# Kernel optimization log

Hardware: AMD Instinct MI355X
Metric: run time of the kernel (lower is better)

The kernel has to match this reference:

```python
import jax, jax.numpy as jnp
import numpy as np

N_NODES = 50000
N_EDGES = 800000
IN, HID, OUT = 512, 256, 128


def spmm(edge_src, edge_dst, edge_weight, x, n_nodes):
    # y[i] = sum_{e: dst[e]==i} w[e] * x[src[e]]   (sparse adjacency @ x)
    msgs = edge_weight[:, None] * x[edge_src]          # [E, F] gather
    return jax.ops.segment_sum(msgs, edge_dst, num_segments=n_nodes)


def setup_inputs() -> dict:
    key = jax.random.key(0)
    k1, k2, k3, k4, k5, k6 = jax.random.split(key, 6)
    features = jax.random.normal(k1, (N_NODES, IN), dtype=jnp.float32)
    edge_src = jax.random.randint(k2, (N_EDGES,), 0, N_NODES, dtype=jnp.int32)
    edge_dst = jax.random.randint(k3, (N_EDGES,), 0, N_NODES, dtype=jnp.int32)
    edge_weight = jax.random.uniform(k4, (N_EDGES,), dtype=jnp.float32)
    # init like torch: uniform(-stdv, stdv), stdv = 1/sqrt(out_dim)
    s1 = 1.0 / np.sqrt(HID)
    s2 = 1.0 / np.sqrt(OUT)
    W1 = jax.random.uniform(k5, (IN, HID), dtype=jnp.float32, minval=-s1, maxval=s1)
    W2 = jax.random.uniform(k6, (HID, OUT), dtype=jnp.float32, minval=-s2, maxval=s2)
    return {"features": features, "edge_src": edge_src, "edge_dst": edge_dst,
            "edge_weight": edge_weight, "W1": W1, "W2": W2}


def reference(features, edge_src, edge_dst, edge_weight, W1, W2):
    n = features.shape[0]
    # layer 1: dense GEMM -> SpMM -> ReLU
    hidden = jax.nn.relu(spmm(edge_src, edge_dst, edge_weight, features @ W1, n))
    # layer 2: dense GEMM -> SpMM
    out = spmm(edge_src, edge_dst, edge_weight, hidden @ W2, n)
    return out
```

## Files before the change

### kernel.cpp

```cpp
#include <hip/hip_runtime.h>

#define NN 50000
#define NE 800000
#define FIN 512
#define FHID 256
#define FOUT 128
#define MPAD 50048

#define TW1_BLOCKS  512
#define TW2_BLOCKS  128

#define NBKT   196
#define BCAP   5120
#define BSTRIDE 16
#define PA_BLOCKS 392
#define E_CHA    2048
#define PB_BLOCKS 196

using bf16x8 = __attribute__((ext_vector_type(8))) short;
using f32x4  = __attribute__((ext_vector_type(4))) float;
using u16x8  = __attribute__((ext_vector_type(8))) unsigned short;

__device__ __forceinline__ unsigned short f2bf(float f) {
    unsigned int u = __builtin_bit_cast(unsigned int, f);
    unsigned int r = (u + 0x7FFFu + ((u >> 16) & 1u)) >> 16;
    return (unsigned short)r;
}
__device__ __forceinline__ float bf2f(unsigned short u) {
    return __builtin_bit_cast(float, (unsigned int)u << 16);
}
__device__ __forceinline__ void gload_lds16(const void* g, void* l) {
    __builtin_amdgcn_global_load_lds(
        (const __attribute__((address_space(1))) void*)g,
        (__attribute__((address_space(3))) void*)l, 16, 0, 0);
}


__global__ __launch_bounds__(256) void fused_passa_prep_kernel(
    const int* __restrict__ src, const int* __restrict__ dst,
    const float* __restrict__ w, int* __restrict__ bcur, int2* __restrict__ barr,
    const float* __restrict__ W1, unsigned short* __restrict__ W1T,
    const float* __restrict__ W2, unsigned short* __restrict__ W2T) {
    int b = blockIdx.x, tid = threadIdx.x;
    if (b < PA_BLOCKS) {
        __shared__ int hist[NBKT];
        __shared__ int resv[NBKT];
        if (tid < NBKT) hist[tid] = 0;
        __syncthreads();
        int base = b * E_CHA + tid;
        int  d[8];
        bool m[8];
#pragma unroll
        for (int j = 0; j < 8; ++j) {
            int e = base + j * 256;
            m[j] = e < NE;
            d[j] = m[j] ? dst[e] : 0;
        }
#pragma unroll
        for (int j = 0; j < 8; ++j)
            if (m[j]) atomicAdd(&hist[d[j] >> 8], 1);
        __syncthreads();
        if (tid < NBKT) {
            int h = hist[tid];
            resv[tid] = (h > 0) ? atomicAdd(&bcur[tid * BSTRIDE], h) : 0;
            hist[tid] = 0;
        }
        __syncthreads();
        int   s[8];
        float wv[8];
#pragma unroll
        for (int j = 0; j < 8; ++j) {
            int e = base + j * 256;
            s[j]  = m[j] ? src[e] : 0;
            wv[j] = m[j] ? w[e] : 0.f;
        }
#pragma unroll
        for (int j = 0; j < 8; ++j) {
            if (m[j]) {
                int bb = d[j] >> 8;
                int r  = atomicAdd(&hist[bb], 1);
                int pos = resv[bb] + r;
                if (pos < BCAP)
                    barr[(size_t)bb * BCAP + pos] =
                        make_int2(s[j] | ((d[j] & 255) << 16), __float_as_int(wv[j]));
            }
        }
    } else if (b < PA_BLOCKS + TW1_BLOCKS) {
        int t = (b - PA_BLOCKS) * 256 + tid;
        int n = t % FHID, k = t / FHID;
        W1T[(size_t)n * FIN + k] = f2bf(W1[t]);
    } else {
        int t = (b - PA_BLOCKS - TW1_BLOCKS) * 256 + tid;
        int n = t % FOUT, k = t / FOUT;
        W2T[(size_t)n * FHID + k] = f2bf(W2[t]);
    }
}


__device__ __forceinline__ void gemm1_body(const float* __restrict__ X,
                                           const unsigned short* __restrict__ BT,
                                           unsigned short* __restrict__ C,
                                           int bx) {
    __shared__ unsigned short As[64 * 64];
    __shared__ unsigned short Bs[256 * 64];

    const int tid  = threadIdx.x;
    const int lane = tid & 63;
    const int wid  = tid >> 6;
    const int brow = bx * 64;
    const int r15   = lane & 15;
    const int khalf = (lane >> 4) * 8;

    const int arow0 = tid >> 3;
    const int arow1 = 32 + (tid >> 3);
    const int acol  = (tid & 7) * 8;
    const int g0 = min(brow + arow0, NN - 1);
    const int g1 = min(brow + arow1, NN - 1);
    const float4* ap0 = (const float4*)(X + (size_t)g0 * FIN + acol);
    const float4* ap1 = (const float4*)(X + (size_t)g1 * FIN + acol);
    const int ab0 = arow0 * 128 + ((acol * 2) ^ ((arow0 & 7) << 4));
    const int ab1 = arow1 * 128 + ((acol * 2) ^ ((arow1 & 7) << 4));

    f32x4 acc[4][4] = {};
    float4 a00 = ap0[0], a01 = ap0[1], a10 = ap1[0], a11 = ap1[1];

#pragma unroll
    for (int k = 0; k < 8; ++k) {
        const int k0 = k * 64;
#pragma unroll
        for (int c = 0; c < 8; ++c) {
            int b   = wid * 8192 + c * 1024 + lane * 16;
            int row = b >> 7;
            int cby = (b & 127) ^ ((row & 7) << 4);
            const char* gb = (const char*)(BT + (size_t)row * FIN + k0) + cby;
            gload_lds16(gb, (char*)Bs + wid * 8192 + c * 1024);
        }
        {
            u16x8 v;
            v[0] = f2bf(a00.x); v[1] = f2bf(a00.y); v[2] = f2bf(a00.z); v[3] = f2bf(a00.w);
            v[4] = f2bf(a01.x); v[5] = f2bf(a01.y); v[6] = f2bf(a01.z); v[7] = f2bf(a01.w);
            *(u16x8*)((char*)As + ab0) = v;
            v[0] = f2bf(a10.x); v[1] = f2bf(a10.y); v[2] = f2bf(a10.z); v[3] = f2bf(a10.w);
            v[4] = f2bf(a11.x); v[5] = f2bf(a11.y); v[6] = f2bf(a11.z); v[7] = f2bf(a11.w);
            *(u16x8*)((char*)As + ab1) = v;
        }
        __syncthreads();

        if (k < 7) {
            int q = (k0 + 64) >> 2;
            a00 = ap0[q]; a01 = ap0[q + 1]; a10 = ap1[q]; a11 = ap1[q + 1];
        }

        bf16x8 bfr[4][2];
#pragma unroll
        for (int n = 0; n < 4; ++n) {
            int row = wid * 64 + n * 16 + r15;
            int rb  = row * 128;
            int sw  = (row & 7) << 4;
#pragma unroll
            for (int ks = 0; ks < 2; ++ks)
                bfr[n][ks] = *(const bf16x8*)((const char*)Bs + rb + (((ks * 32 + khalf) * 2) ^ sw));
        }
#pragma unroll
        for (int m = 0; m < 4; ++m) {
            int row = m * 16 + r15;
            int rb  = row * 128;
            int sw  = (row & 7) << 4;
            bf16x8 af0 = *(const bf16x8*)((const char*)As + rb + (((0 + khalf) * 2) ^ sw));
            bf16x8 af1 = *(const bf16x8*)((const char*)As + rb + (((32 + khalf) * 2) ^ sw));
#pragma unroll
            for (int n = 0; n < 4; ++n) {
                acc[m][n] = __builtin_amdgcn_mfma_f32_16x16x32_bf16(af0, bfr[n][0], acc[m][n], 0, 0, 0);
                acc[m][n] = __builtin_amdgcn_mfma_f32_16x16x32_bf16(af1, bfr[n][1], acc[m][n], 0, 0, 0);
            }
        }
        __syncthreads();
    }

    const int rsub = (lane >> 4) * 4;
#pragma unroll
    for (int m = 0; m < 4; ++m) {
#pragma unroll
        for (int r = 0; r < 4; ++r) {
            int grow = brow + m * 16 + rsub + r;
            if (grow < NN) {
#pragma unroll
                for (int n = 0; n < 4; ++n)
                    C[(size_t)grow * FHID + wid * 64 + n * 16 + r15] = f2bf(acc[m][n][r]);
            }
        }
    }
}


__device__ __forceinline__ void passb_body(const int2* __restrict__ barr,
                                           const int* __restrict__ bcur,
                                           int* __restrict__ off,
                                           int2* __restrict__ csr) {
    __shared__ int sc[256];
    __shared__ int cnt[256];
    __shared__ int pre[256];
    __shared__ int wsum[4];
    int b = blockIdx.x, tid = threadIdx.x, lane = tid & 63, wid = tid >> 6;

    int v = (tid < NBKT) ? min(bcur[tid * BSTRIDE], BCAP) : 0;
    int s = v;
#pragma unroll
    for (int d = 1; d < 64; d <<= 1) {
        int t = __shfl_up(s, d, 64);
        if (lane >= d) s += t;
    }
    if (lane == 63) wsum[wid] = s;
    __syncthreads();
    int wo = 0;
#pragma unroll
    for (int j = 0; j < 4; ++j)
        if (j < wid) wo += wsum[j];
    sc[tid] = wo + s - v;
    if (b == 0 && tid == NBKT - 1) off[NN] = wo + s;
    cnt[tid] = 0;
    __syncthreads();

    int bko_b = sc[b];
    int total = min(bcur[b * BSTRIDE], BCAP);
    const int2* seg = barr + (size_t)b * BCAP;

    for (int k = tid; k < total; k += 256)
        atomicAdd(&cnt[(seg[k].x >> 16) & 255], 1);
    __syncthreads();
    int v2 = cnt[tid];
    int s2 = v2;
#pragma unroll
    for (int d = 1; d < 64; d <<= 1) {
        int t = __shfl_up(s2, d, 64);
        if (lane >= d) s2 += t;
    }
    if (lane == 63) wsum[wid] = s2;
    __syncthreads();
    int wo2 = 0;
#pragma unroll
    for (int j = 0; j < 4; ++j)
        if (j < wid) wo2 += wsum[j];
    int base = bko_b + wo2 + s2 - v2;
    pre[tid] = base;
    int n = b * 256 + tid;
    if (n < NN) off[n] = base;
    cnt[tid] = 0;
    __syncthreads();
    for (int k = tid; k < total; k += 256) {
        int2 pl = seg[k];
        int dlow = (pl.x >> 16) & 255;
        int r = atomicAdd(&cnt[dlow], 1);
        csr[pre[dlow] + r] = make_int2(pl.x & 0xFFFF, pl.y);
    }
}


__global__ __launch_bounds__(256) void fused_passb_gemm1_kernel(
    const int2* __restrict__ barr, const int* __restrict__ bcur,
    int* __restrict__ off, int2* __restrict__ csr,
    const float* __restrict__ X, const unsigned short* __restrict__ BT,
    unsigned short* __restrict__ C) {
    if (blockIdx.x < PB_BLOCKS) {
        passb_body(barr, bcur, off, csr);
    } else {
        gemm1_body(X, BT, C, blockIdx.x - PB_BLOCKS);
    }
}


__global__ __launch_bounds__(256) void spmm_pair_kernel(const unsigned short* __restrict__ X,
                                                        const int* __restrict__ off,
                                                        const int2* __restrict__ csr,
                                                        unsigned short* __restrict__ Y) {
    int wave = (int)((blockIdx.x * 256 + threadIdx.x) >> 6);
    int lane = threadIdx.x & 63;
    int half = lane >> 5;
    int hl   = lane & 31;
    int n = wave * 2 + half;
    if (n >= NN) return;
    int e0 = off[n];
    int e1 = off[n + 1];

    float acc[8] = {};
    for (int e = e0; e < e1; e += 8) {
        unsigned ssb[8];
        float    ww[8];
#pragma unroll
        for (int j = 0; j < 8; ++j) {
            int  ee = e + j;
            bool v  = ee < e1;
            int2 sw = csr[v ? ee : e0];
            ssb[j] = (unsigned)(sw.x * (FHID * 2));
            ww[j]  = v ? __int_as_float(sw.y) : 0.f;
        }
        u16x8 r[8];
#pragma unroll
        for (int j = 0; j < 8; ++j)
            r[j] = *(const u16x8*)((const char*)X + ssb[j] + hl * 16);
#pragma unroll
        for (int j = 0; j < 8; ++j)
#pragma unroll
            for (int k = 0; k < 8; ++k)
                acc[k] += ww[j] * bf2f(r[j][k]);
    }
    u16x8 o;
#pragma unroll
    for (int k = 0; k < 8; ++k) o[k] = f2bf(fmaxf(acc[k], 0.f));
    *(u16x8*)(Y + (size_t)n * FHID + (size_t)hl * 8) = o;
}


__global__ __launch_bounds__(256) void gemm2_kernel(const unsigned short* __restrict__ A,
                                                    const unsigned short* __restrict__ BT,
                                                    unsigned short* __restrict__ C) {
    __shared__ unsigned short As[64 * 64];
    __shared__ unsigned short Bs[128 * 64];

    const int tid  = threadIdx.x;
    const int lane = tid & 63;
    const int wid  = tid >> 6;
    const int brow = blockIdx.x * 64;
    const int r15   = lane & 15;
    const int khalf = (lane >> 4) * 8;

    f32x4 acc[4][2] = {};

#pragma unroll
    for (int k = 0; k < 4; ++k) {
        const int k0 = k * 64;
#pragma unroll
        for (int c = 0; c < 4; ++c) {
            int b   = wid * 4096 + c * 1024 + lane * 16;
            int row = b >> 7;
            int cby = (b & 127) ^ ((row & 7) << 4);
            const char* gb = (const char*)(BT + (size_t)row * FHID + k0) + cby;
            gload_lds16(gb, (char*)Bs + wid * 4096 + c * 1024);
        }
#pragma unroll
        for (int c = 0; c < 2; ++c) {
            int b   = wid * 2048 + c * 1024 + lane * 16;
            int row = b >> 7;
            int cby = (b & 127) ^ ((row & 7) << 4);
            const char* ga = (const char*)(A + (size_t)(brow + row) * FHID + k0) + cby;
            gload_lds16(ga, (char*)As + wid * 2048 + c * 1024);
        }
        __syncthreads();

        bf16x8 bfr[2][2];
#pragma unroll
        for (int n = 0; n < 2; ++n) {
            int row = wid * 32 + n * 16 + r15;
            int rb  = row * 128;
            int sw  = (row & 7) << 4;
#pragma unroll
            for (int ks = 0; ks < 2; ++ks)
                bfr[n][ks] = *(const bf16x8*)((const char*)Bs + rb + (((ks * 32 + khalf) * 2) ^ sw));
        }
#pragma unroll
        for (int m = 0; m < 4; ++m) {
            int row = m * 16 + r15;
            int rb  = row * 128;
            int sw  = (row & 7) << 4;
            bf16x8 af0 = *(const bf16x8*)((const char*)As + rb + (((0 + khalf) * 2) ^ sw));
            bf16x8 af1 = *(const bf16x8*)((const char*)As + rb + (((32 + khalf) * 2) ^ sw));
#pragma unroll
            for (int n = 0; n < 2; ++n) {
                acc[m][n] = __builtin_amdgcn_mfma_f32_16x16x32_bf16(af0, bfr[n][0], acc[m][n], 0, 0, 0);
                acc[m][n] = __builtin_amdgcn_mfma_f32_16x16x32_bf16(af1, bfr[n][1], acc[m][n], 0, 0, 0);
            }
        }
        __syncthreads();
    }

    const int rsub = (lane >> 4) * 4;
#pragma unroll
    for (int m = 0; m < 4; ++m) {
#pragma unroll
        for (int r = 0; r < 4; ++r) {
            int grow = brow + m * 16 + rsub + r;
            if (grow < NN) {
#pragma unroll
                for (int n = 0; n < 2; ++n)
                    C[(size_t)grow * FOUT + wid * 32 + n * 16 + r15] = f2bf(acc[m][n][r]);
            }
        }
    }
}


__global__ __launch_bounds__(256) void spmm_quad_kernel(const unsigned short* __restrict__ X,
                                                        const int* __restrict__ off,
                                                        const int2* __restrict__ csr,
                                                        float* __restrict__ Y) {
    int wave = (int)((blockIdx.x * 256 + threadIdx.x) >> 6);
    int lane = threadIdx.x & 63;
    int q  = lane >> 4;
    int hl = lane & 15;
    int n = wave * 4 + q;
    if (n >= NN) return;
    int e0 = off[n];
    int e1 = off[n + 1];

    float acc[8] = {};
    for (int e = e0; e < e1; e += 8) {
        unsigned ssb[8];
        float    ww[8];
#pragma unroll
        for (int j = 0; j < 8; ++j) {
            int  ee = e + j;
            bool v  = ee < e1;
            int2 sw = csr[v ? ee : e0];
            ssb[j] = (unsigned)(sw.x * (FOUT * 2));
            ww[j]  = v ? __int_as_float(sw.y) : 0.f;
        }
        u16x8 r[8];
#pragma unroll
        for (int j = 0; j < 8; ++j)
            r[j] = *(const u16x8*)((const char*)X + ssb[j] + hl * 16);
#pragma unroll
        for (int j = 0; j < 8; ++j)
#pragma unroll
            for (int k = 0; k < 8; ++k)
                acc[k] += ww[j] * bf2f(r[j][k]);
    }
    float4 o0 = make_float4(acc[0], acc[1], acc[2], acc[3]);
    float4 o1 = make_float4(acc[4], acc[5], acc[6], acc[7]);
    *(float4*)(Y + (size_t)n * FOUT + hl * 8) = o0;
    *(float4*)(Y + (size_t)n * FOUT + hl * 8 + 4) = o1;
}


extern "C" void kernel_launch(void* const* d_in, const int* in_sizes, int n_in,
                              void* d_out, int out_size, void* d_ws, size_t ws_size,
                              hipStream_t stream) {
    const float* features = (const float*)d_in[0];
    const int*   edge_src = (const int*)d_in[1];
    const int*   edge_dst = (const int*)d_in[2];
    const float* edge_w   = (const float*)d_in[3];
    const float* W1       = (const float*)d_in[4];
    const float* W2       = (const float*)d_in[5];
    float* out = (float*)d_out;

    char*  ws  = (char*)d_ws;
    size_t ofs = 0;
    auto carve = [&](size_t bytes) -> void* {
        void* r = ws + ofs;
        ofs = (ofs + bytes + 255) & ~(size_t)255;
        return r;
    };
    int*            off   = (int*)carve((NN + 1) * sizeof(int));
    int*            bcur  = (int*)carve(NBKT * BSTRIDE * sizeof(int));
    int2*           barr  = (int2*)carve((size_t)NBKT * BCAP * sizeof(int2));
    int2*           csr   = (int2*)carve((size_t)NE * sizeof(int2));
    unsigned short* W1T   = (unsigned short*)carve((size_t)FHID * FIN * 2);
    unsigned short* W2T   = (unsigned short*)carve((size_t)FOUT * FHID * 2);
    unsigned short* H0b   = (unsigned short*)carve((size_t)MPAD * FHID * 2);
    unsigned short* Hb    = (unsigned short*)carve((size_t)MPAD * FHID * 2);
    unsigned short* H1b   = H0b;

    hipMemsetAsync(bcur, 0, NBKT * BSTRIDE * sizeof(int), stream);

    fused_passa_prep_kernel<<<PA_BLOCKS + TW1_BLOCKS + TW2_BLOCKS, 256, 0, stream>>>(
        edge_src, edge_dst, edge_w, bcur, barr, W1, W1T, W2, W2T);

    fused_passb_gemm1_kernel<<<PB_BLOCKS + MPAD / 64, 256, 0, stream>>>(
        barr, bcur, off, csr, features, W1T, H0b);

    spmm_pair_kernel<<<6250, 256, 0, stream>>>(H0b, off, csr, Hb);

    gemm2_kernel<<<MPAD / 64, 256, 0, stream>>>(Hb, W2T, H1b);

    spmm_quad_kernel<<<3125, 256, 0, stream>>>(H1b, off, csr, out);
}
```

Before: 169.6 us.

## Split GEMM1 into column halves with 512-thread blocks and widen pass B

GEMM1 now uses a 64x128 output tile per 512-thread block, with eight waves each computing a 64x16 strip, so there are twice as many blocks covering the 256 output columns. Pass B is adapted to run with 512 threads per block, using the extra threads in its edge-scatter loops. The aim is more waves in flight and smaller per-wave accumulator state. In exchange, each fp32 feature row is read and converted to bf16 twice, once per column half. The register prefetch of the next A tile is also removed, so global loads are no longer overlapped with the MFMA work.

```diff
diff --git a/kernel.cpp b/kernel.cpp
--- a/kernel.cpp
+++ b/kernel.cpp
@@ -16,6 +16,8 @@
 #define PA_BLOCKS 392
 #define E_CHA    2048
 #define PB_BLOCKS 196
+
+#define GEMM1_BLOCKS 1564
 
 using bf16x8 = __attribute__((ext_vector_type(8))) short;
 using f32x4  = __attribute__((ext_vector_type(4))) float;
@@ -100,79 +102,63 @@
 __device__ __forceinline__ void gemm1_body(const float* __restrict__ X,
                                            const unsigned short* __restrict__ BT,
                                            unsigned short* __restrict__ C,
-                                           int bx) {
+                                           int bx, int by) {
     __shared__ unsigned short As[64 * 64];
-    __shared__ unsigned short Bs[256 * 64];
+    __shared__ unsigned short Bs[128 * 64];
 
     const int tid  = threadIdx.x;
     const int lane = tid & 63;
-    const int wid  = tid >> 6;
+    const int wv   = tid >> 6;
     const int brow = bx * 64;
+    const int bcol = by * 128;
     const int r15   = lane & 15;
     const int khalf = (lane >> 4) * 8;
 
-    const int arow0 = tid >> 3;
-    const int arow1 = 32 + (tid >> 3);
-    const int acol  = (tid & 7) * 8;
-    const int g0 = min(brow + arow0, NN - 1);
-    const int g1 = min(brow + arow1, NN - 1);
-    const float4* ap0 = (const float4*)(X + (size_t)g0 * FIN + acol);
-    const float4* ap1 = (const float4*)(X + (size_t)g1 * FIN + acol);
-    const int ab0 = arow0 * 128 + ((acol * 2) ^ ((arow0 & 7) << 4));
-    const int ab1 = arow1 * 128 + ((acol * 2) ^ ((arow1 & 7) << 4));
-
-    f32x4 acc[4][4] = {};
-    float4 a00 = ap0[0], a01 = ap0[1], a10 = ap1[0], a11 = ap1[1];
+    const int arow = tid >> 3;
+    const int acol = (tid & 7) * 8;
+    const int grow_a = min(brow + arow, NN - 1);
+    const float4* ap = (const float4*)(X + (size_t)grow_a * FIN + acol);
+    const int ab = arow * 128 + ((acol * 2) ^ ((arow & 7) << 4));
+
+    f32x4 acc[4] = {};
 
 #pragma unroll
     for (int k = 0; k < 8; ++k) {
         const int k0 = k * 64;
 #pragma unroll
-        for (int c = 0; c < 8; ++c) {
-            int b   = wid * 8192 + c * 1024 + lane * 16;
+        for (int c = 0; c < 2; ++c) {
+            int b   = c * 8192 + tid * 16;
             int row = b >> 7;
             int cby = (b & 127) ^ ((row & 7) << 4);
-            const char* gb = (const char*)(BT + (size_t)row * FIN + k0) + cby;
-            gload_lds16(gb, (char*)Bs + wid * 8192 + c * 1024);
+            const char* gb = (const char*)(BT + (size_t)(bcol + row) * FIN + k0) + cby;
+            gload_lds16(gb, (char*)Bs + b);
         }
         {
+            float4 a0 = ap[k0 >> 2], a1 = ap[(k0 >> 2) + 1];
             u16x8 v;
-            v[0] = f2bf(a00.x); v[1] = f2bf(a00.y); v[2] = f2bf(a00.z); v[3] = f2bf(a00.w);
-            v[4] = f2bf(a01.x); v[5] = f2bf(a01.y); v[6] = f2bf(a01.z); v[7] = f2bf(a01.w);
-            *(u16x8*)((char*)As + ab0) = v;
-            v[0] = f2bf(a10.x); v[1] = f2bf(a10.y); v[2] = f2bf(a10.z); v[3] = f2bf(a10.w);
-            v[4] = f2bf(a11.x); v[5] = f2bf(a11.y); v[6] = f2bf(a11.z); v[7] = f2bf(a11.w);
-            *(u16x8*)((char*)As + ab1) = v;
-        }
-        __syncthreads();
-
-        if (k < 7) {
-            int q = (k0 + 64) >> 2;
-            a00 = ap0[q]; a01 = ap0[q + 1]; a10 = ap1[q]; a11 = ap1[q + 1];
-        }
-
-        bf16x8 bfr[4][2];
-#pragma unroll
-        for (int n = 0; n < 4; ++n) {
-            int row = wid * 64 + n * 16 + r15;
+            v[0] = f2bf(a0.x); v[1] = f2bf(a0.y); v[2] = f2bf(a0.z); v[3] = f2bf(a0.w);
+            v[4] = f2bf(a1.x); v[5] = f2bf(a1.y); v[6] = f2bf(a1.z); v[7] = f2bf(a1.w);
+            *(u16x8*)((char*)As + ab) = v;
+        }
+        __syncthreads();
+
+        bf16x8 bfr0, bfr1;
+        {
+            int row = wv * 16 + r15;
             int rb  = row * 128;
             int sw  = (row & 7) << 4;
-#pragma unroll
-            for (int ks = 0; ks < 2; ++ks)
-                bfr[n][ks] = *(const bf16x8*)((const char*)Bs + rb + (((ks * 32 + khalf) * 2) ^ sw));
+            bfr0 = *(const bf16x8*)((const char*)Bs + rb + (((0  + khalf) * 2) ^ sw));
+            bfr1 = *(const bf16x8*)((const char*)Bs + rb + (((32 + khalf) * 2) ^ sw));
         }
 #pragma unroll
         for (int m = 0; m < 4; ++m) {
             int row = m * 16 + r15;
             int rb  = row * 128;
             int sw  = (row & 7) << 4;
-            bf16x8 af0 = *(const bf16x8*)((const char*)As + rb + (((0 + khalf) * 2) ^ sw));
+            bf16x8 af0 = *(const bf16x8*)((const char*)As + rb + (((0  + khalf) * 2) ^ sw));
             bf16x8 af1 = *(const bf16x8*)((const char*)As + rb + (((32 + khalf) * 2) ^ sw));
-#pragma unroll
-            for (int n = 0; n < 4; ++n) {
-                acc[m][n] = __builtin_amdgcn_mfma_f32_16x16x32_bf16(af0, bfr[n][0], acc[m][n], 0, 0, 0);
-                acc[m][n] = __builtin_amdgcn_mfma_f32_16x16x32_bf16(af1, bfr[n][1], acc[m][n], 0, 0, 0);
-            }
+            acc[m] = __builtin_amdgcn_mfma_f32_16x16x32_bf16(af0, bfr0, acc[m], 0, 0, 0);
+            acc[m] = __builtin_amdgcn_mfma_f32_16x16x32_bf16(af1, bfr1, acc[m], 0, 0, 0);
         }
         __syncthreads();
     }
@@ -183,20 +169,17 @@
 #pragma unroll
         for (int r = 0; r < 4; ++r) {
             int grow = brow + m * 16 + rsub + r;
-            if (grow < NN) {
-#pragma unroll
-                for (int n = 0; n < 4; ++n)
-                    C[(size_t)grow * FHID + wid * 64 + n * 16 + r15] = f2bf(acc[m][n][r]);
-            }
-        }
-    }
-}
-
-
-__device__ __forceinline__ void passb_body(const int2* __restrict__ barr,
-                                           const int* __restrict__ bcur,
-                                           int* __restrict__ off,
-                                           int2* __restrict__ csr) {
+            if (grow < NN)
+                C[(size_t)grow * FHID + bcol + wv * 16 + r15] = f2bf(acc[m][r]);
+        }
+    }
+}
+
+
+__device__ __forceinline__ void passb_body512(const int2* __restrict__ barr,
+                                              const int* __restrict__ bcur,
+                                              int* __restrict__ off,
+                                              int2* __restrict__ csr) {
     __shared__ int sc[256];
     __shared__ int cnt[256];
     __shared__ int pre[256];
@@ -210,44 +193,48 @@
         int t = __shfl_up(s, d, 64);
         if (lane >= d) s += t;
     }
-    if (lane == 63) wsum[wid] = s;
+    if (wid < 4 && lane == 63) wsum[wid] = s;
     __syncthreads();
-    int wo = 0;
-#pragma unroll
-    for (int j = 0; j < 4; ++j)
-        if (j < wid) wo += wsum[j];
-    sc[tid] = wo + s - v;
-    if (b == 0 && tid == NBKT - 1) off[NN] = wo + s;
-    cnt[tid] = 0;
+    if (tid < 256) {
+        int wo = 0;
+#pragma unroll
+        for (int j = 0; j < 4; ++j)
+            if (j < wid) wo += wsum[j];
+        sc[tid] = wo + s - v;
+        if (b == 0 && tid == NBKT - 1) off[NN] = wo + s;
+        cnt[tid] = 0;
+    }
     __syncthreads();
 
     int bko_b = sc[b];
     int total = min(bcur[b * BSTRIDE], BCAP);
     const int2* seg = barr + (size_t)b * BCAP;
 
-    for (int k = tid; k < total; k += 256)
+    for (int k = tid; k < total; k += 512)
         atomicAdd(&cnt[(seg[k].x >> 16) & 255], 1);
     __syncthreads();
-    int v2 = cnt[tid];
+    int v2 = (tid < 256) ? cnt[tid] : 0;
     int s2 = v2;
 #pragma unroll
     for (int d = 1; d < 64; d <<= 1) {
         int t = __shfl_up(s2, d, 64);
         if (lane >= d) s2 += t;
     }
-    if (lane == 63) wsum[wid] = s2;
+    if (wid < 4 && lane == 63) wsum[wid] = s2;
     __syncthreads();
-    int wo2 = 0;
-#pragma unroll
-    for (int j = 0; j < 4; ++j)
-        if (j < wid) wo2 += wsum[j];
-    int base = bko_b + wo2 + s2 - v2;
-    pre[tid] = base;
-    int n = b * 256 + tid;
-    if (n < NN) off[n] = base;
-    cnt[tid] = 0;
+    if (tid < 256) {
+        int wo2 = 0;
+#pragma unroll
+        for (int j = 0; j < 4; ++j)
+            if (j < wid) wo2 += wsum[j];
+        int base = bko_b + wo2 + s2 - v2;
+        pre[tid] = base;
+        int n = b * 256 + tid;
+        if (n < NN) off[n] = base;
+        cnt[tid] = 0;
+    }
     __syncthreads();
-    for (int k = tid; k < total; k += 256) {
+    for (int k = tid; k < total; k += 512) {
         int2 pl = seg[k];
         int dlow = (pl.x >> 16) & 255;
         int r = atomicAdd(&cnt[dlow], 1);
@@ -256,15 +243,16 @@
 }
 
 
-__global__ __launch_bounds__(256) void fused_passb_gemm1_kernel(
+__global__ __launch_bounds__(512) void fused_passb_gemm1_kernel(
     const int2* __restrict__ barr, const int* __restrict__ bcur,
     int* __restrict__ off, int2* __restrict__ csr,
     const float* __restrict__ X, const unsigned short* __restrict__ BT,
     unsigned short* __restrict__ C) {
     if (blockIdx.x < PB_BLOCKS) {
-        passb_body(barr, bcur, off, csr);
+        passb_body512(barr, bcur, off, csr);
     } else {
-        gemm1_body(X, BT, C, blockIdx.x - PB_BLOCKS);
+        int g = blockIdx.x - PB_BLOCKS;
+        gemm1_body(X, BT, C, g >> 1, g & 1);
     }
 }
 
@@ -464,7 +452,7 @@
     fused_passa_prep_kernel<<<PA_BLOCKS + TW1_BLOCKS + TW2_BLOCKS, 256, 0, stream>>>(
         edge_src, edge_dst, edge_w, bcur, barr, W1, W1T, W2, W2T);
 
-    fused_passb_gemm1_kernel<<<PB_BLOCKS + MPAD / 64, 256, 0, stream>>>(
+    fused_passb_gemm1_kernel<<<PB_BLOCKS + GEMM1_BLOCKS, 512, 0, stream>>>(
         barr, bcur, off, csr, features, W1T, H0b);
 
     spmm_pair_kernel<<<6250, 256, 0, stream>>>(H0b, off, csr, Hb);
```

After: 175.8 us. 3.6% more time.

## Stage full A row-block in LDS and read W1T directly from global in GEMM1

Applied to the files above, without the earlier changes.

The first GEMM now converts the whole 64x512 fp32 feature block to bf16 into a 64 KB LDS buffer in one pass with a single barrier. The loop over K then runs with no further syncs. The B operand (transposed W1) is no longer staged through LDS; each wave loads its MFMA fragments straight from global memory, relying on cache hits since W1T is small and shared by all blocks. This removes the per-K-step barriers and LDS staging of B. In exchange it uses more LDS per block, which may lower occupancy, and adds uncoalesced global loads of B on the MFMA critical path.

```diff
diff --git a/kernel.cpp b/kernel.cpp
--- a/kernel.cpp
+++ b/kernel.cpp
@@ -101,80 +101,53 @@
                                            const unsigned short* __restrict__ BT,
                                            unsigned short* __restrict__ C,
                                            int bx) {
-    __shared__ unsigned short As[64 * 64];
-    __shared__ unsigned short Bs[256 * 64];
+    __shared__ unsigned short As[64 * 512];
 
     const int tid  = threadIdx.x;
     const int lane = tid & 63;
-    const int wid  = tid >> 6;
+    const int wv   = tid >> 6;
     const int brow = bx * 64;
     const int r15   = lane & 15;
     const int khalf = (lane >> 4) * 8;
 
-    const int arow0 = tid >> 3;
-    const int arow1 = 32 + (tid >> 3);
-    const int acol  = (tid & 7) * 8;
-    const int g0 = min(brow + arow0, NN - 1);
-    const int g1 = min(brow + arow1, NN - 1);
-    const float4* ap0 = (const float4*)(X + (size_t)g0 * FIN + acol);
-    const float4* ap1 = (const float4*)(X + (size_t)g1 * FIN + acol);
-    const int ab0 = arow0 * 128 + ((acol * 2) ^ ((arow0 & 7) << 4));
-    const int ab1 = arow1 * 128 + ((acol * 2) ^ ((arow1 & 7) << 4));
+#pragma unroll
+    for (int g = 0; g < 16; ++g) {
+        int idx  = g * 256 + tid;
+        int row  = idx >> 6;
+        int col0 = (idx & 63) * 8;
+        int grow = min(brow + row, NN - 1);
+        const float4* p = (const float4*)(X + (size_t)grow * FIN + col0);
+        float4 a0 = p[0], a1 = p[1];
+        u16x8 v;
+        v[0] = f2bf(a0.x); v[1] = f2bf(a0.y); v[2] = f2bf(a0.z); v[3] = f2bf(a0.w);
+        v[4] = f2bf(a1.x); v[5] = f2bf(a1.y); v[6] = f2bf(a1.z); v[7] = f2bf(a1.w);
+        int byte = row * 1024 + ((col0 * 2) ^ ((row & 7) << 4));
+        *(u16x8*)((char*)As + byte) = v;
+    }
+    __syncthreads();
 
     f32x4 acc[4][4] = {};
-    float4 a00 = ap0[0], a01 = ap0[1], a10 = ap1[0], a11 = ap1[1];
-
-#pragma unroll
-    for (int k = 0; k < 8; ++k) {
-        const int k0 = k * 64;
-#pragma unroll
-        for (int c = 0; c < 8; ++c) {
-            int b   = wid * 8192 + c * 1024 + lane * 16;
-            int row = b >> 7;
-            int cby = (b & 127) ^ ((row & 7) << 4);
-            const char* gb = (const char*)(BT + (size_t)row * FIN + k0) + cby;
-            gload_lds16(gb, (char*)Bs + wid * 8192 + c * 1024);
-        }
-        {
-            u16x8 v;
-            v[0] = f2bf(a00.x); v[1] = f2bf(a00.y); v[2] = f2bf(a00.z); v[3] = f2bf(a00.w);
-            v[4] = f2bf(a01.x); v[5] = f2bf(a01.y); v[6] = f2bf(a01.z); v[7] = f2bf(a01.w);
-            *(u16x8*)((char*)As + ab0) = v;
-            v[0] = f2bf(a10.x); v[1] = f2bf(a10.y); v[2] = f2bf(a10.z); v[3] = f2bf(a10.w);
-            v[4] = f2bf(a11.x); v[5] = f2bf(a11.y); v[6] = f2bf(a11.z); v[7] = f2bf(a11.w);
-            *(u16x8*)((char*)As + ab1) = v;
-        }
-        __syncthreads();
-
-        if (k < 7) {
-            int q = (k0 + 64) >> 2;
-            a00 = ap0[q]; a01 = ap0[q + 1]; a10 = ap1[q]; a11 = ap1[q + 1];
-        }
-
-        bf16x8 bfr[4][2];
+#pragma unroll
+    for (int ks = 0; ks < 16; ++ks) {
+        bf16x8 bfr[4];
 #pragma unroll
         for (int n = 0; n < 4; ++n) {
-            int row = wid * 64 + n * 16 + r15;
-            int rb  = row * 128;
-            int sw  = (row & 7) << 4;
-#pragma unroll
-            for (int ks = 0; ks < 2; ++ks)
-                bfr[n][ks] = *(const bf16x8*)((const char*)Bs + rb + (((ks * 32 + khalf) * 2) ^ sw));
-        }
+            int wrow = wv * 64 + n * 16 + r15;
+            bfr[n] = *(const bf16x8*)(BT + (size_t)wrow * FIN + ks * 32 + khalf);
+        }
+        bf16x8 af[4];
 #pragma unroll
         for (int m = 0; m < 4; ++m) {
-            int row = m * 16 + r15;
-            int rb  = row * 128;
-            int sw  = (row & 7) << 4;
-            bf16x8 af0 = *(const bf16x8*)((const char*)As + rb + (((0 + khalf) * 2) ^ sw));
-            bf16x8 af1 = *(const bf16x8*)((const char*)As + rb + (((32 + khalf) * 2) ^ sw));
-#pragma unroll
-            for (int n = 0; n < 4; ++n) {
-                acc[m][n] = __builtin_amdgcn_mfma_f32_16x16x32_bf16(af0, bfr[n][0], acc[m][n], 0, 0, 0);
-                acc[m][n] = __builtin_amdgcn_mfma_f32_16x16x32_bf16(af1, bfr[n][1], acc[m][n], 0, 0, 0);
-            }
-        }
-        __syncthreads();
+            int row  = m * 16 + r15;
+            int byte = row * 1024 + (((ks * 32 + khalf) * 2) ^ ((row & 7) << 4));
+            af[m] = *(const bf16x8*)((const char*)As + byte);
+        }
+#pragma unroll
+        for (int m = 0; m < 4; ++m)
+#pragma unroll
+            for (int n = 0; n < 4; ++n)
+                acc[m][n] = __builtin_amdgcn_mfma_f32_16x16x32_bf16(
+                    af[m], bfr[n], acc[m][n], 0, 0, 0);
     }
 
     const int rsub = (lane >> 4) * 4;
@@ -186,7 +159,7 @@
             if (grow < NN) {
 #pragma unroll
                 for (int n = 0; n < 4; ++n)
-                    C[(size_t)grow * FHID + wid * 64 + n * 16 + r15] = f2bf(acc[m][n][r]);
+                    C[(size_t)grow * FHID + wv * 64 + n * 16 + r15] = f2bf(acc[m][n][r]);
             }
         }
     }
```

Measured after the change: 183.4 us. 8.2% more time.
